# Kernel tuning notes

Measured on AMD Instinct MI355X. Metric: run time of the kernel, lower is better.

## Reference

```python
import jax, jax.numpy as jnp
import numpy as np

# tanh-approximate GELU, matching F.gelu(..., approximate='tanh')
_SQRT_2_OVER_PI = 0.7978845608028654

def gelu_tanh(x):
    return 0.5 * x * (1.0 + jnp.tanh(_SQRT_2_OVER_PI * (x + 0.044715 * x * x * x)))

def setup_inputs() -> dict:
    key = jax.random.key(0)
    k1, k2, k3 = jax.random.split(key, 3)
    E, T, H, F = 8, 2048, 1024, 4096
    x = jax.random.normal(k1, (E, T, H), dtype=jnp.float32)
    w1 = jax.random.normal(k2, (E, H, F), dtype=jnp.float32) * (1.0 / np.sqrt(H))
    w2 = jax.random.normal(k3, (E, F, H), dtype=jnp.float32) * (1.0 / np.sqrt(F))
    return {"x": x, "w1": w1, "w2": w2}

def reference(x, w1, w2):
    # [E,T,H] @ [E,H,F] -> [E,T,F]
    h = jnp.einsum('eth,ehf->etf', x, w1)
    h = gelu_tanh(h)
    # [E,T,F] @ [E,F,H] -> [E,T,H]
    return jnp.einsum('etf,efh->eth', h, w2)
```

## Files before the change

kernel.cpp:

```cpp
#include <hip/hip_runtime.h>
#include <hip/hip_bf16.h>

typedef __attribute__((ext_vector_type(8))) short short8;
typedef __attribute__((ext_vector_type(4))) float f32x4;

typedef const __attribute__((address_space(1))) void* as1cv_t;
typedef __attribute__((address_space(3))) void* as3v_t;
typedef __attribute__((address_space(3))) const char* as3cc_t;
typedef __attribute__((address_space(3))) const short8* as3s8_t;

__device__ __forceinline__ unsigned short f2bf(float f) {
    unsigned u = __float_as_uint(f);
    u += 0x7fffu + ((u >> 16) & 1u);
    return (unsigned short)(u >> 16);
}

__device__ __forceinline__ float gelu_tanh_f(float x) {
    float t = 0.7978845608028654f * (x + 0.044715f * x * x * x);
    float u = 2.0f * t;
    u = fminf(fmaxf(u, -30.0f), 30.0f);
    float e = __expf(u);
    float th = (e - 1.0f) / (e + 1.0f);
    return 0.5f * x * (1.0f + th);
}

__global__ void cvt_f32_to_bf16(const float* __restrict__ in,
                                unsigned short* __restrict__ out,
                                long long n) {
    long long i = (long long)blockIdx.x * blockDim.x + threadIdx.x;
    long long stride = (long long)gridDim.x * blockDim.x;
    const float4* in4 = (const float4*)in;
    ushort4* out4 = (ushort4*)out;
    long long n4 = n >> 2;
    for (long long j = i; j < n4; j += stride) {
        float4 v = in4[j];
        ushort4 o;
        o.x = f2bf(v.x); o.y = f2bf(v.y); o.z = f2bf(v.z); o.w = f2bf(v.w);
        out4[j] = o;
    }
}

__global__ void transpose_cvt64(const float* __restrict__ in,
                                unsigned short* __restrict__ out,
                                int R, int C) {
    __shared__ float t[64][65];
    int e = blockIdx.z;
    int c0 = blockIdx.x * 64;
    int r0 = blockIdx.y * 64;
    const float* ine = in + (size_t)e * R * C;
    unsigned short* oute = out + (size_t)e * R * C;
    int tid = threadIdx.x;
    int lx = tid & 15, ly = tid >> 4;
#pragma unroll
    for (int i = 0; i < 4; i++) {
        float4 v = *(const float4*)(ine + (size_t)(r0 + ly + i * 16) * C + c0 + lx * 4);
        t[lx * 4 + 0][ly + i * 16] = v.x;
        t[lx * 4 + 1][ly + i * 16] = v.y;
        t[lx * 4 + 2][ly + i * 16] = v.z;
        t[lx * 4 + 3][ly + i * 16] = v.w;
    }
    __syncthreads();
#pragma unroll
    for (int i = 0; i < 4; i++) {
        int c = ly + i * 16;
        ushort4 o;
        o.x = f2bf(t[c][lx * 4 + 0]);
        o.y = f2bf(t[c][lx * 4 + 1]);
        o.z = f2bf(t[c][lx * 4 + 2]);
        o.w = f2bf(t[c][lx * 4 + 3]);
        *(ushort4*)(oute + (size_t)(c0 + c) * R + r0 + lx * 4) = o;
    }
}

__device__ __forceinline__ void gload16(const void* g, void* l) {
    __builtin_amdgcn_global_load_lds((as1cv_t)g, (as3v_t)l, 16, 0, 0);
}

#define MFMA_BF16 __builtin_amdgcn_mfma_f32_16x16x32_bf16

template <int DO_GELU>
__global__ __launch_bounds__(512, 2) void gemm8p(
    const unsigned short* __restrict__ A,
    const unsigned short* __restrict__ Bt,
    void* __restrict__ Cout,
    int M, int N, int K, int tiles_m, int per_e, int nwg)
{
    int bid = blockIdx.x;
    int gbid = (bid & 7) * (nwg >> 3) + (bid >> 3);
    int e  = gbid / per_e;
    int t0_ = gbid % per_e;
    int bn = t0_ / tiles_m;
    int bm = t0_ % tiles_m;

    const size_t K2 = (size_t)K * 2;
    const char* Ae = (const char*)A  + ((size_t)e * M * K + (size_t)bm * 256 * K) * 2;
    const char* Be = (const char*)Bt + ((size_t)e * N * K + (size_t)bn * 256 * K) * 2;

    __shared__ alignas(16) unsigned short lds[2 * 32768];
    char* ldsc = (char*)lds;
    as3cc_t lb = (as3cc_t)(const char*)lds;

    int tid  = threadIdx.x;
    int wid  = tid >> 6;
    int lane = tid & 63;
    int wave_m = wid >> 2;
    int wave_n = wid & 3;

    int srow = wid * 8 + (lane >> 3);
    int kbsw = ((lane & 7) ^ (srow & 7)) << 4;
    const char* gA = Ae + (size_t)srow * K2 + kbsw;
    const char* gB = Be + (size_t)srow * K2 + kbsw;
    const size_t HROW = 64 * K2;
    const size_t HALF = 128 * K2;
    int sOff = wid << 10;

    unsigned kg   = (unsigned)(lane >> 4);
    unsigned keyl = (unsigned)(lane & 7) & 7u;
    keyl = (unsigned)((lane & 15) & 7);
    unsigned sl0  = (kg ^ keyl) << 4;
    unsigned aoff = (unsigned)(wave_m * 16384 + (lane & 15) * 128) + sl0;
    unsigned boff = 32768u + (unsigned)((wave_n >> 1) * 16384 +
                    ((wave_n & 1) * 64 + (lane & 15)) * 128) + sl0;

    f32x4 acc[8][4];
    f32x4 zero = {0.0f, 0.0f, 0.0f, 0.0f};
#pragma unroll
    for (int i = 0; i < 8; i++)
#pragma unroll
        for (int j = 0; j < 4; j++) acc[i][j] = zero;

    int NT = K >> 6;

#define STG_A(h, r, bufbit) gload16(gA + (h) * HALF + (r) * HROW, \
        ldsc + ((bufbit) << 16) + (h) * 16384 + (r) * 8192 + sOff)
#define STG_B(h, r, bufbit) gload16(gB + (h) * HALF + (r) * HROW, \
        ldsc + ((bufbit) << 16) + 32768 + (h) * 16384 + (r) * 8192 + sOff)

    STG_A(0, 0, 0); STG_A(0, 1, 0); STG_A(1, 0, 0); STG_A(1, 1, 0);
    STG_B(0, 0, 0); STG_B(0, 1, 0); STG_B(1, 0, 0); STG_B(1, 1, 0);
    gB += 128;
    if (NT > 1) {
        STG_B(0, 0, 1); STG_B(0, 1, 1); STG_B(1, 0, 1); STG_B(1, 1, 1);
        asm volatile("s_waitcnt vmcnt(4)" ::: "memory");
    } else {
        asm volatile("s_waitcnt vmcnt(0)" ::: "memory");
    }
    gB += 128;
    gA += 128;
    __builtin_amdgcn_s_barrier();

    for (int t = 0; t < NT; ++t) {
        unsigned bufR = (unsigned)(t & 1) << 16;
        int wbA = (t + 1) & 1;
        int wbB = t & 1;
        bool stA = (t + 1) < NT;
        bool stB = (t + 2) < NT;

        unsigned pa0 = bufR + aoff, pa1 = pa0 ^ 64u;
        unsigned pb0 = bufR + boff, pb1 = pb0 ^ 64u;

        short8 aL[4][2], aH[4][2], bL[2][2], bH[2][2];

#pragma unroll
        for (int mi = 0; mi < 4; ++mi) {
            aL[mi][0] = *(as3s8_t)(lb + (pa0 + mi * 2048));
            aL[mi][1] = *(as3s8_t)(lb + (pa1 + mi * 2048));
        }
#pragma unroll
        for (int ni = 0; ni < 2; ++ni) {
            bL[ni][0] = *(as3s8_t)(lb + (pb0 + ni * 2048));
            bL[ni][1] = *(as3s8_t)(lb + (pb1 + ni * 2048));
        }
        if (stA) { STG_A(0, 0, wbA); STG_A(0, 1, wbA); }
        __builtin_amdgcn_sched_barrier(0);
        __builtin_amdgcn_s_barrier();
        __builtin_amdgcn_s_setprio(1);
#pragma unroll
        for (int ks = 0; ks < 2; ++ks)
#pragma unroll
            for (int mi = 0; mi < 4; ++mi)
#pragma unroll
                for (int ni = 0; ni < 2; ++ni)
                    acc[mi][ni] = MFMA_BF16(aL[mi][ks], bL[ni][ks], acc[mi][ni], 0, 0, 0);
        __builtin_amdgcn_s_setprio(0);
        __builtin_amdgcn_sched_barrier(0);
        __builtin_amdgcn_s_barrier();

#pragma unroll
        for (int ni = 0; ni < 2; ++ni) {
            bH[ni][0] = *(as3s8_t)(lb + (pb0 + (2 + ni) * 2048));
            bH[ni][1] = *(as3s8_t)(lb + (pb1 + (2 + ni) * 2048));
        }
        if (stA) { STG_A(1, 0, wbA); STG_A(1, 1, wbA); }
        gA += 128;
        __builtin_amdgcn_sched_barrier(0);
        __builtin_amdgcn_s_barrier();
        __builtin_amdgcn_s_setprio(1);
#pragma unroll
        for (int ks = 0; ks < 2; ++ks)
#pragma unroll
            for (int mi = 0; mi < 4; ++mi)
#pragma unroll
                for (int ni = 0; ni < 2; ++ni)
                    acc[mi][2 + ni] = MFMA_BF16(aL[mi][ks], bH[ni][ks], acc[mi][2 + ni], 0, 0, 0);
        __builtin_amdgcn_s_setprio(0);
        __builtin_amdgcn_sched_barrier(0);
        __builtin_amdgcn_s_barrier();

#pragma unroll
        for (int mi = 0; mi < 4; ++mi) {
            aH[mi][0] = *(as3s8_t)(lb + (pa0 + (4 + mi) * 2048));
            aH[mi][1] = *(as3s8_t)(lb + (pa1 + (4 + mi) * 2048));
        }
        if (stB) { STG_B(0, 0, wbB); STG_B(0, 1, wbB); }
        __builtin_amdgcn_sched_barrier(0);
        __builtin_amdgcn_s_barrier();
        __builtin_amdgcn_s_setprio(1);
#pragma unroll
        for (int ks = 0; ks < 2; ++ks)
#pragma unroll
            for (int mi = 0; mi < 4; ++mi)
#pragma unroll
                for (int ni = 0; ni < 2; ++ni)
                    acc[4 + mi][2 + ni] = MFMA_BF16(aH[mi][ks], bH[ni][ks], acc[4 + mi][2 + ni], 0, 0, 0);
        __builtin_amdgcn_s_setprio(0);
        __builtin_amdgcn_sched_barrier(0);
        __builtin_amdgcn_s_barrier();

        if (stB) { STG_B(1, 0, wbB); STG_B(1, 1, wbB); }
        gB += 128;
        if (stB) asm volatile("s_waitcnt vmcnt(4)" ::: "memory");
        else     asm volatile("s_waitcnt vmcnt(0)" ::: "memory");
        __builtin_amdgcn_sched_barrier(0);
        __builtin_amdgcn_s_barrier();
        __builtin_amdgcn_s_setprio(1);
#pragma unroll
        for (int ks = 0; ks < 2; ++ks)
#pragma unroll
            for (int mi = 0; mi < 4; ++mi)
#pragma unroll
                for (int ni = 0; ni < 2; ++ni)
                    acc[4 + mi][ni] = MFMA_BF16(aH[mi][ks], bL[ni][ks], acc[4 + mi][ni], 0, 0, 0);
        __builtin_amdgcn_s_setprio(0);
        __builtin_amdgcn_sched_barrier(0);
        __builtin_amdgcn_s_barrier();
    }
#undef STG_A
#undef STG_B

    int row0 = bm * 256 + wave_m * 128 + ((lane >> 4) << 2);
    int col0 = bn * 256 + wave_n * 64 + (lane & 15);
    if (DO_GELU) {
        unsigned short* Ce = (unsigned short*)Cout + (size_t)e * M * N;
#pragma unroll
        for (int m = 0; m < 8; ++m)
#pragma unroll
            for (int n = 0; n < 4; ++n)
#pragma unroll
                for (int j = 0; j < 4; ++j) {
                    int row = row0 + m * 16 + j;
                    int col = col0 + n * 16;
                    Ce[(size_t)row * N + col] = f2bf(gelu_tanh_f(acc[m][n][j]));
                }
    } else {
        float* Ce = (float*)Cout + (size_t)e * M * N;
#pragma unroll
        for (int m = 0; m < 8; ++m)
#pragma unroll
            for (int n = 0; n < 4; ++n)
#pragma unroll
                for (int j = 0; j < 4; ++j) {
                    int row = row0 + m * 16 + j;
                    int col = col0 + n * 16;
                    Ce[(size_t)row * N + col] = acc[m][n][j];
                }
    }
}

extern "C" void kernel_launch(void* const* d_in, const int* in_sizes, int n_in,
                              void* d_out, int out_size, void* d_ws, size_t ws_size,
                              hipStream_t stream) {
    const float* x  = (const float*)d_in[0];
    const float* w1 = (const float*)d_in[1];
    const float* w2 = (const float*)d_in[2];
    float* out = (float*)d_out;

    const int E = 8, T = 2048, H = 1024, F = 4096;

    unsigned short* xb  = (unsigned short*)d_ws;
    unsigned short* w1t = xb  + (size_t)E * T * H;
    unsigned short* w2t = w1t + (size_t)E * H * F;
    unsigned short* hb  = w2t + (size_t)E * F * H;

    cvt_f32_to_bf16<<<2048, 256, 0, stream>>>(x, xb, (long long)E * T * H);

    transpose_cvt64<<<dim3(F / 64, H / 64, E), 256, 0, stream>>>(w1, w1t, H, F);
    transpose_cvt64<<<dim3(H / 64, F / 64, E), 256, 0, stream>>>(w2, w2t, F, H);

    {
        int M = T, N = F, K = H;
        int tiles_m = M / 256, per_e = tiles_m * (N / 256);
        int nwg = E * per_e;
        gemm8p<1><<<nwg, 512, 0, stream>>>(xb, w1t, hb, M, N, K, tiles_m, per_e, nwg);
    }
    {
        int M = T, N = H, K = F;
        int tiles_m = M / 256, per_e = tiles_m * (N / 256);
        int nwg = E * per_e;
        gemm8p<0><<<nwg, 512, 0, stream>>>(hb, w2t, out, M, N, K, tiles_m, per_e, nwg);
    }
}
```

Baseline: 389.7 us.

## Make first GEMM process four M-tiles per workgroup with continuous K pipeline

The first GEMM kernel now has each workgroup iterate over four consecutive 256-row M tiles for the same N tile. The K-loop software pipeline runs continuously across tile boundaries, and the epilogue is written out inside the loop before the accumulators are reset. This aims to hide prologue and pipeline-drain costs and to reuse B tiles through cache. It reduces grid size, which may leave CUs underused, and it adds branching and register pressure in the main loop.

```diff
diff --git a/kernel.cpp b/kernel.cpp
--- a/kernel.cpp
+++ b/kernel.cpp
@@ -78,23 +78,24 @@
 
 #define MFMA_BF16 __builtin_amdgcn_mfma_f32_16x16x32_bf16
 
-template <int DO_GELU>
-__global__ __launch_bounds__(512, 2) void gemm8p(
+template <int DO_GELU, int ROUNDS>
+__device__ __forceinline__ void gemm_body(
     const unsigned short* __restrict__ A,
     const unsigned short* __restrict__ Bt,
     void* __restrict__ Cout,
-    int M, int N, int K, int tiles_m, int per_e, int nwg)
+    int M, int N, int K, int bmw_count, int per_e, int nwg)
 {
     int bid = blockIdx.x;
     int gbid = (bid & 7) * (nwg >> 3) + (bid >> 3);
     int e  = gbid / per_e;
     int t0_ = gbid % per_e;
-    int bn = t0_ / tiles_m;
-    int bm = t0_ % tiles_m;
+    int bn  = t0_ / bmw_count;
+    int sub = t0_ % bmw_count;
+    int bm0 = sub * ROUNDS;
 
     const size_t K2 = (size_t)K * 2;
-    const char* Ae = (const char*)A  + ((size_t)e * M * K + (size_t)bm * 256 * K) * 2;
-    const char* Be = (const char*)Bt + ((size_t)e * N * K + (size_t)bn * 256 * K) * 2;
+    const char* Ae = (const char*)A  + ((size_t)e * M * K + (size_t)bm0 * 256 * K) * 2;
+    const char* Be = (const char*)Bt + ((size_t)e * N * K + (size_t)bn  * 256 * K) * 2;
 
     __shared__ alignas(16) unsigned short lds[2 * 32768];
     char* ldsc = (char*)lds;
@@ -115,8 +116,7 @@
     int sOff = wid << 10;
 
     unsigned kg   = (unsigned)(lane >> 4);
-    unsigned keyl = (unsigned)(lane & 7) & 7u;
-    keyl = (unsigned)((lane & 15) & 7);
+    unsigned keyl = (unsigned)((lane & 15) & 7);
     unsigned sl0  = (kg ^ keyl) << 4;
     unsigned aoff = (unsigned)(wave_m * 16384 + (lane & 15) * 128) + sl0;
     unsigned boff = 32768u + (unsigned)((wave_n >> 1) * 16384 +
@@ -129,7 +129,13 @@
 #pragma unroll
         for (int j = 0; j < 4; j++) acc[i][j] = zero;
 
-    int NT = K >> 6;
+    const int KT = K >> 6;
+    const int NT_TOT = ROUNDS * KT;
+    const size_t AROUND = 255 * K2;
+
+    int kA = 0, kB = 0;
+#define ADV_A() do { gA += 128; if (++kA == KT) { kA = 0; gA += AROUND; } } while (0)
+#define ADV_B() do { gB += 128; if (++kB == KT) { kB = 0; gB -= K2; } } while (0)
 
 #define STG_A(h, r, bufbit) gload16(gA + (h) * HALF + (r) * HROW, \
         ldsc + ((bufbit) << 16) + (h) * 16384 + (r) * 8192 + sOff)
@@ -138,23 +144,25 @@
 
     STG_A(0, 0, 0); STG_A(0, 1, 0); STG_A(1, 0, 0); STG_A(1, 1, 0);
     STG_B(0, 0, 0); STG_B(0, 1, 0); STG_B(1, 0, 0); STG_B(1, 1, 0);
-    gB += 128;
-    if (NT > 1) {
+    ADV_B();
+    if (NT_TOT > 1) {
         STG_B(0, 0, 1); STG_B(0, 1, 1); STG_B(1, 0, 1); STG_B(1, 1, 1);
         asm volatile("s_waitcnt vmcnt(4)" ::: "memory");
     } else {
         asm volatile("s_waitcnt vmcnt(0)" ::: "memory");
     }
-    gB += 128;
-    gA += 128;
+    ADV_B();
+    ADV_A();
     __builtin_amdgcn_s_barrier();
 
-    for (int t = 0; t < NT; ++t) {
+    int ktEp = 0, rEp = 0;
+
+    for (int t = 0; t < NT_TOT; ++t) {
         unsigned bufR = (unsigned)(t & 1) << 16;
         int wbA = (t + 1) & 1;
         int wbB = t & 1;
-        bool stA = (t + 1) < NT;
-        bool stB = (t + 2) < NT;
+        bool stA = (t + 1) < NT_TOT;
+        bool stB = (t + 2) < NT_TOT;
 
         unsigned pa0 = bufR + aoff, pa1 = pa0 ^ 64u;
         unsigned pb0 = bufR + boff, pb1 = pb0 ^ 64u;
@@ -192,7 +200,7 @@
             bH[ni][1] = *(as3s8_t)(lb + (pb1 + (2 + ni) * 2048));
         }
         if (stA) { STG_A(1, 0, wbA); STG_A(1, 1, wbA); }
-        gA += 128;
+        ADV_A();
         __builtin_amdgcn_sched_barrier(0);
         __builtin_amdgcn_s_barrier();
         __builtin_amdgcn_s_setprio(1);
@@ -228,7 +236,7 @@
         __builtin_amdgcn_s_barrier();
 
         if (stB) { STG_B(1, 0, wbB); STG_B(1, 1, wbB); }
-        gB += 128;
+        ADV_B();
         if (stB) asm volatile("s_waitcnt vmcnt(4)" ::: "memory");
         else     asm volatile("s_waitcnt vmcnt(0)" ::: "memory");
         __builtin_amdgcn_sched_barrier(0);
@@ -244,37 +252,58 @@
         __builtin_amdgcn_s_setprio(0);
         __builtin_amdgcn_sched_barrier(0);
         __builtin_amdgcn_s_barrier();
+
+        if (++ktEp == KT) {
+            ktEp = 0;
+            int row0 = (bm0 + rEp) * 256 + wave_m * 128 + ((lane >> 4) << 2);
+            int col0 = bn * 256 + wave_n * 64 + (lane & 15);
+            if (DO_GELU) {
+                unsigned short* Ce = (unsigned short*)Cout + (size_t)e * M * N;
+#pragma unroll
+                for (int m = 0; m < 8; ++m)
+#pragma unroll
+                    for (int n = 0; n < 4; ++n)
+#pragma unroll
+                        for (int j = 0; j < 4; ++j) {
+                            int row = row0 + m * 16 + j;
+                            int col = col0 + n * 16;
+                            Ce[(size_t)row * N + col] = f2bf(gelu_tanh_f(acc[m][n][j]));
+                        }
+            } else {
+                float* Ce = (float*)Cout + (size_t)e * M * N;
+#pragma unroll
+                for (int m = 0; m < 8; ++m)
+#pragma unroll
+                    for (int n = 0; n < 4; ++n)
+#pragma unroll
+                        for (int j = 0; j < 4; ++j) {
+                            int row = row0 + m * 16 + j;
+                            int col = col0 + n * 16;
+                            Ce[(size_t)row * N + col] = acc[m][n][j];
+                        }
+            }
+            rEp++;
+#pragma unroll
+            for (int i = 0; i < 8; i++)
+#pragma unroll
+                for (int j = 0; j < 4; j++) acc[i][j] = zero;
+        }
     }
 #undef STG_A
 #undef STG_B
-
-    int row0 = bm * 256 + wave_m * 128 + ((lane >> 4) << 2);
-    int col0 = bn * 256 + wave_n * 64 + (lane & 15);
-    if (DO_GELU) {
-        unsigned short* Ce = (unsigned short*)Cout + (size_t)e * M * N;
-#pragma unroll
-        for (int m = 0; m < 8; ++m)
-#pragma unroll
-            for (int n = 0; n < 4; ++n)
-#pragma unroll
-                for (int j = 0; j < 4; ++j) {
-                    int row = row0 + m * 16 + j;
-                    int col = col0 + n * 16;
-                    Ce[(size_t)row * N + col] = f2bf(gelu_tanh_f(acc[m][n][j]));
-                }
-    } else {
-        float* Ce = (float*)Cout + (size_t)e * M * N;
-#pragma unroll
-        for (int m = 0; m < 8; ++m)
-#pragma unroll
-            for (int n = 0; n < 4; ++n)
-#pragma unroll
-                for (int j = 0; j < 4; ++j) {
-                    int row = row0 + m * 16 + j;
-                    int col = col0 + n * 16;
-                    Ce[(size_t)row * N + col] = acc[m][n][j];
-                }
-    }
+#undef ADV_A
+#undef ADV_B
+}
+
+__global__ __launch_bounds__(512, 2) void gemm_mlp1(
+    const unsigned short* __restrict__ A, const unsigned short* __restrict__ Bt,
+    void* __restrict__ C, int M, int N, int K, int bmw, int per_e, int nwg) {
+    gemm_body<1, 4>(A, Bt, C, M, N, K, bmw, per_e, nwg);
+}
+__global__ __launch_bounds__(512, 2) void gemm_mlp2(
+    const unsigned short* __restrict__ A, const unsigned short* __restrict__ Bt,
+    void* __restrict__ C, int M, int N, int K, int bmw, int per_e, int nwg) {
+    gemm_body<0, 1>(A, Bt, C, M, N, K, bmw, per_e, nwg);
 }
 
 extern "C" void kernel_launch(void* const* d_in, const int* in_sizes, int n_in,
@@ -298,15 +327,17 @@
     transpose_cvt64<<<dim3(H / 64, F / 64, E), 256, 0, stream>>>(w2, w2t, F, H);
 
     {
-        int M = T, N = F, K = H;
-        int tiles_m = M / 256, per_e = tiles_m * (N / 256);
+        int M_ = T, N_ = F, K_ = H;
+        int bmw = (M_ / 256) / 4;
+        int per_e = (N_ / 256) * bmw;
         int nwg = E * per_e;
-        gemm8p<1><<<nwg, 512, 0, stream>>>(xb, w1t, hb, M, N, K, tiles_m, per_e, nwg);
+        gemm_mlp1<<<nwg, 512, 0, stream>>>(xb, w1t, hb, M_, N_, K_, bmw, per_e, nwg);
     }
     {
-        int M = T, N = H, K = F;
-        int tiles_m = M / 256, per_e = tiles_m * (N / 256);
+        int M_ = T, N_ = H, K_ = F;
+        int bmw = M_ / 256;
+        int per_e = (N_ / 256) * bmw;
         int nwg = E * per_e;
-        gemm8p<0><<<nwg, 512, 0, stream>>>(hb, w2t, out, M, N, K, tiles_m, per_e, nwg);
-    }
-}
+        gemm_mlp2<<<nwg, 512, 0, stream>>>(hb, w2t, out, M_, N_, K_, bmw, per_e, nwg);
+    }
+}
```

Measured after the change: 386.8 us. Within noise of the previous version (-0.7%).
